# Kernel tuning notes

Measured on AMD Instinct MI355X. Metric: run time of the kernel, lower is better.

Reference implementation:

```python
import jax, jax.numpy as jnp
import numpy as np

VOCAB, EMB, HID = 128, 10, 20


def setup_inputs() -> dict:
    key = jax.random.key(0)
    ks = jax.random.split(key, 8)
    B, T = 256, 2048
    inputs = jax.random.randint(ks[0], (B, T), 0, VOCAB)
    s_emb = 1.0
    s_ih = 1.0 / np.sqrt(HID)  # torch RNN init: U(-1/sqrt(H), 1/sqrt(H))
    emb = jax.random.normal(ks[1], (VOCAB, EMB), dtype=jnp.float32)
    W_ih = jax.random.uniform(ks[2], (HID, EMB), jnp.float32, -s_ih, s_ih)
    W_hh = jax.random.uniform(ks[3], (HID, HID), jnp.float32, -s_ih, s_ih)
    b_ih = jax.random.uniform(ks[4], (HID,), jnp.float32, -s_ih, s_ih)
    b_hh = jax.random.uniform(ks[5], (HID,), jnp.float32, -s_ih, s_ih)
    s_out = 1.0 / np.sqrt(HID)
    W_out = jax.random.uniform(ks[6], (VOCAB, HID), jnp.float32, -s_out, s_out)
    b_out = jax.random.uniform(ks[7], (VOCAB,), jnp.float32, -s_out, s_out)
    return {"inputs": inputs, "emb": emb, "W_ih": W_ih, "W_hh": W_hh,
            "b_ih": b_ih, "b_hh": b_hh, "W_out": W_out, "b_out": b_out}


def reference(inputs, emb, W_ih, W_hh, b_ih, b_hh, W_out, b_out):
    # embedding lookup: [B, T, EMB]
    x = emb[inputs]
    B = x.shape[0]
    # precompute input contribution for all timesteps: [B, T, HID]
    xW = jnp.einsum('bte,he->bth', x, W_ih) + b_ih + b_hh
    xW_t = jnp.swapaxes(xW, 0, 1)  # [T, B, HID] for scan over time

    def step(h, xw_t):
        h = jnp.tanh(xw_t + h @ W_hh.T)
        return h, h

    h0 = jnp.zeros((B, HID), dtype=x.dtype)
    _, hs = jax.lax.scan(step, h0, xW_t)  # hs: [T, B, HID]
    hs = jnp.swapaxes(hs, 0, 1)  # [B, T, HID]
    # final linear projection: [B, T, VOCAB]
    return jnp.einsum('bth,vh->btv', hs, W_out) + b_out
```

## Files before the change

kernel.cpp:

```cpp
#include <hip/hip_runtime.h>

#define VOCAB 128
#define EMB   10
#define HID   20
#define BATCH 256
#define TLEN  2048
#define PRESCALE 2.8853900817779268f

__global__ __launch_bounds__(256)
void build_table(const float* __restrict__ emb, const float* __restrict__ W_ih,
                 const float* __restrict__ W_hh,
                 const float* __restrict__ b_ih, const float* __restrict__ b_hh,
                 float* __restrict__ P) {
    int idx = blockIdx.x * blockDim.x + threadIdx.x;
    if (idx < VOCAB * HID) {
        int v = idx / HID, j = idx % HID;
        float acc = b_ih[j] + b_hh[j];
        #pragma unroll
        for (int e = 0; e < EMB; ++e)
            acc = fmaf(W_ih[j * EMB + e], emb[v * EMB + e], acc);
        float wsum = 0.f;
        #pragma unroll
        for (int k = 0; k < HID; ++k) wsum += W_hh[j * HID + k];
        P[idx] = (acc + wsum) * PRESCALE;
    }
}

#define RNN_STEP(XW) { \
    const int ri_ = __float_as_int(r); \
    float bc[HID]; \
    _Pragma("unroll") \
    for (int k = 0; k < HID; ++k) \
        bc[k] = __int_as_float(__builtin_amdgcn_readlane(ri_, k)); \
    float a0 = (XW), a1 = 0.f, a2 = 0.f, a3 = 0.f; \
    _Pragma("unroll") \
    for (int k = 0; k < HID; k += 4) { \
        a0 = fmaf(w[k + 0], bc[k + 0], a0); \
        a1 = fmaf(w[k + 1], bc[k + 1], a1); \
        a2 = fmaf(w[k + 2], bc[k + 2], a2); \
        a3 = fmaf(w[k + 3], bc[k + 3], a3); } \
    float z_ = (a0 + a1) + (a2 + a3); \
    float u_ = __builtin_amdgcn_exp2f(z_); \
    r = __builtin_amdgcn_rcpf(u_ + 1.0f); }

__global__ __launch_bounds__(256)
void rnn_fused(const int* __restrict__ tokens, const float* __restrict__ W_hh,
               const float* __restrict__ P, const float* __restrict__ W_out,
               const float* __restrict__ b_out, float* __restrict__ out) {
    __shared__ float Pl[VOCAB * HID];
    __shared__ __align__(16) int tok[TLEN + 16];
    __shared__ float hbuf[2][64][64];
    const int tid  = threadIdx.x;
    const int lane = tid & 63;
    const int wid  = tid >> 6;
    const int b    = blockIdx.x;

    for (int i = tid; i < VOCAB * HID; i += 256) Pl[i] = P[i];
    const int4* src = (const int4*)(tokens + (size_t)b * TLEN);
    int4* dst = (int4*)tok;
    for (int i = tid; i < TLEN / 4; i += 256) dst[i] = src[i];
    if (tid < 16) tok[TLEN + tid] = 0;

    const int j = (lane & 31) < HID ? (lane & 31) : HID - 1;
    float w[HID], wB[HID];
    float bo0 = 0.f, bo1 = 0.f;
    if (wid == 0) {
        #pragma unroll
        for (int k = 0; k < HID; ++k)
            w[k] = W_hh[j * HID + k] * (-2.0f * PRESCALE);
    } else {
        const int v0 = 2 * lane, v1 = 2 * lane + 1;
        float s0 = 0.f, s1 = 0.f;
        #pragma unroll
        for (int k = 0; k < HID; ++k) {
            float wa = W_out[v0 * HID + k], wb = W_out[v1 * HID + k];
            s0 += wa; s1 += wb;
            w[k]  = -2.0f * wa;
            wB[k] = -2.0f * wb;
        }
        bo0 = b_out[v0] + s0; bo1 = b_out[v1] + s1;
    }
    __syncthreads();

    float r = 0.5f;
    int4 ta, tb, tkc, tkd;
    float xw0[4], xw1[4];
    if (wid == 0) {
        __builtin_amdgcn_s_setprio(1);
        ta  = *(const int4*)&tok[0];
        tb  = *(const int4*)&tok[4];
        tkc = *(const int4*)&tok[8];
        tkd = *(const int4*)&tok[12];
        xw0[0] = Pl[ta.x * HID + j]; xw0[1] = Pl[ta.y * HID + j];
        xw0[2] = Pl[ta.z * HID + j]; xw0[3] = Pl[ta.w * HID + j];
        xw1[0] = Pl[tb.x * HID + j]; xw1[1] = Pl[tb.y * HID + j];
        xw1[2] = Pl[tb.z * HID + j]; xw1[3] = Pl[tb.w * HID + j];
    }

    for (int c = 0; c < 33; ++c) {
        if (wid == 0 && c < 32) {
            float* hb = &hbuf[c & 1][0][lane];
            for (int t8 = 0; t8 < 64; t8 += 8) {
                const int t = c * 64 + t8;
                float* hrow = hb + t8 * 64;
                RNN_STEP(xw0[0]); hrow[0 * 64] = r;
                RNN_STEP(xw0[1]); hrow[1 * 64] = r;
                RNN_STEP(xw0[2]); hrow[2 * 64] = r;
                RNN_STEP(xw0[3]); hrow[3 * 64] = r;
                float n0[4] = {Pl[tkc.x * HID + j], Pl[tkc.y * HID + j],
                               Pl[tkc.z * HID + j], Pl[tkc.w * HID + j]};
                tkc = *(const int4*)&tok[t + 16];
                RNN_STEP(xw1[0]); hrow[4 * 64] = r;
                RNN_STEP(xw1[1]); hrow[5 * 64] = r;
                RNN_STEP(xw1[2]); hrow[6 * 64] = r;
                RNN_STEP(xw1[3]); hrow[7 * 64] = r;
                float n1[4] = {Pl[tkd.x * HID + j], Pl[tkd.y * HID + j],
                               Pl[tkd.z * HID + j], Pl[tkd.w * HID + j]};
                tkd = *(const int4*)&tok[t + 20];
                #pragma unroll
                for (int u = 0; u < 4; ++u) { xw0[u] = n0[u]; xw1[u] = n1[u]; }
            }
        }
        if (wid > 0 && c > 0) {
            const int cc = c - 1;
            const float* hb = &hbuf[cc & 1][0][0];
            float* outb = out + ((size_t)b * TLEN + (size_t)cc * 64) * VOCAB + 2 * lane;
            for (int rr = wid - 1; rr < 64; rr += 3) {
                const float* hr = hb + rr * 64;
                float a0 = bo0, a1 = bo1;
                #pragma unroll
                for (int k = 0; k < HID; k += 4) {
                    float4 hv = *(const float4*)(hr + k);
                    a0 = fmaf(hv.x, w[k + 0], a0); a1 = fmaf(hv.x, wB[k + 0], a1);
                    a0 = fmaf(hv.y, w[k + 1], a0); a1 = fmaf(hv.y, wB[k + 1], a1);
                    a0 = fmaf(hv.z, w[k + 2], a0); a1 = fmaf(hv.z, wB[k + 2], a1);
                    a0 = fmaf(hv.w, w[k + 3], a0); a1 = fmaf(hv.w, wB[k + 3], a1);
                }
                *(float2*)(outb + (size_t)rr * VOCAB) = make_float2(a0, a1);
            }
        }
        __syncthreads();
    }
}

extern "C" void kernel_launch(void* const* d_in, const int* in_sizes, int n_in,
                              void* d_out, int out_size, void* d_ws, size_t ws_size,
                              hipStream_t stream) {
    const int*   inputs = (const int*)  d_in[0];
    const float* emb    = (const float*)d_in[1];
    const float* W_ih   = (const float*)d_in[2];
    const float* W_hh   = (const float*)d_in[3];
    const float* b_ih   = (const float*)d_in[4];
    const float* b_hh   = (const float*)d_in[5];
    const float* W_out  = (const float*)d_in[6];
    const float* b_out  = (const float*)d_in[7];
    float* out = (float*)d_out;

    float* P = (float*)d_ws;

    build_table<<<(VOCAB * HID + 255) / 256, 256, 0, stream>>>(emb, W_ih, W_hh,
                                                               b_ih, b_hh, P);
    rnn_fused<<<BATCH, 256, 0, stream>>>(inputs, W_hh, P, W_out, b_out, out);
}
```

Baseline: 419.6 us.

## Process two batch rows per block with interleaved dual recurrence in one wave

Each block now handles two sequences. The recurrence wave runs both hidden-state chains interleaved in a single step macro: A is broadcast from lanes 0-19 and B from lanes 32-51. The projection waves cover 128 rows per chunk, and the grid is halved. The goal is to hide the serial step latency through instruction-level parallelism, at the cost of doubling per-step readlane and FMA work and leaving half of the CUs without a block.

```diff
diff --git a/kernel.cpp b/kernel.cpp
--- a/kernel.cpp
+++ b/kernel.cpp
@@ -26,42 +26,56 @@
     }
 }
 
-#define RNN_STEP(XW) { \
-    const int ri_ = __float_as_int(r); \
-    float bc[HID]; \
-    _Pragma("unroll") \
-    for (int k = 0; k < HID; ++k) \
-        bc[k] = __int_as_float(__builtin_amdgcn_readlane(ri_, k)); \
-    float a0 = (XW), a1 = 0.f, a2 = 0.f, a3 = 0.f; \
+#define RNN_STEP2(XWA, XWB) { \
+    const int riA_ = __float_as_int(rA); \
+    const int riB_ = __float_as_int(rB); \
+    float aA0 = (XWA), aA1 = 0.f, aA2 = 0.f, aA3 = 0.f; \
+    float aB0 = (XWB), aB1 = 0.f, aB2 = 0.f, aB3 = 0.f; \
     _Pragma("unroll") \
     for (int k = 0; k < HID; k += 4) { \
-        a0 = fmaf(w[k + 0], bc[k + 0], a0); \
-        a1 = fmaf(w[k + 1], bc[k + 1], a1); \
-        a2 = fmaf(w[k + 2], bc[k + 2], a2); \
-        a3 = fmaf(w[k + 3], bc[k + 3], a3); } \
-    float z_ = (a0 + a1) + (a2 + a3); \
-    float u_ = __builtin_amdgcn_exp2f(z_); \
-    r = __builtin_amdgcn_rcpf(u_ + 1.0f); }
+        float cA0 = __int_as_float(__builtin_amdgcn_readlane(riA_, k + 0)); \
+        float cB0 = __int_as_float(__builtin_amdgcn_readlane(riB_, 32 + k + 0)); \
+        float cA1 = __int_as_float(__builtin_amdgcn_readlane(riA_, k + 1)); \
+        float cB1 = __int_as_float(__builtin_amdgcn_readlane(riB_, 32 + k + 1)); \
+        float cA2 = __int_as_float(__builtin_amdgcn_readlane(riA_, k + 2)); \
+        float cB2 = __int_as_float(__builtin_amdgcn_readlane(riB_, 32 + k + 2)); \
+        float cA3 = __int_as_float(__builtin_amdgcn_readlane(riA_, k + 3)); \
+        float cB3 = __int_as_float(__builtin_amdgcn_readlane(riB_, 32 + k + 3)); \
+        aA0 = fmaf(w[k + 0], cA0, aA0); aB0 = fmaf(w[k + 0], cB0, aB0); \
+        aA1 = fmaf(w[k + 1], cA1, aA1); aB1 = fmaf(w[k + 1], cB1, aB1); \
+        aA2 = fmaf(w[k + 2], cA2, aA2); aB2 = fmaf(w[k + 2], cB2, aB2); \
+        aA3 = fmaf(w[k + 3], cA3, aA3); aB3 = fmaf(w[k + 3], cB3, aB3); } \
+    float zA_ = (aA0 + aA1) + (aA2 + aA3); \
+    float zB_ = (aB0 + aB1) + (aB2 + aB3); \
+    float uA_ = __builtin_amdgcn_exp2f(zA_); \
+    float uB_ = __builtin_amdgcn_exp2f(zB_); \
+    rA = __builtin_amdgcn_rcpf(uA_ + 1.0f); \
+    rB = __builtin_amdgcn_rcpf(uB_ + 1.0f); }
 
 __global__ __launch_bounds__(256)
 void rnn_fused(const int* __restrict__ tokens, const float* __restrict__ W_hh,
                const float* __restrict__ P, const float* __restrict__ W_out,
                const float* __restrict__ b_out, float* __restrict__ out) {
     __shared__ float Pl[VOCAB * HID];
-    __shared__ __align__(16) int tok[TLEN + 16];
+    __shared__ __align__(16) int tokA[TLEN + 16];
+    __shared__ __align__(16) int tokB[TLEN + 16];
     __shared__ float hbuf[2][64][64];
     const int tid  = threadIdx.x;
     const int lane = tid & 63;
     const int wid  = tid >> 6;
-    const int b    = blockIdx.x;
+    const int blk  = blockIdx.x;
+    const int bA   = 2 * blk, bB = 2 * blk + 1;
 
     for (int i = tid; i < VOCAB * HID; i += 256) Pl[i] = P[i];
-    const int4* src = (const int4*)(tokens + (size_t)b * TLEN);
-    int4* dst = (int4*)tok;
-    for (int i = tid; i < TLEN / 4; i += 256) dst[i] = src[i];
-    if (tid < 16) tok[TLEN + tid] = 0;
+    const int4* srcA = (const int4*)(tokens + (size_t)bA * TLEN);
+    const int4* srcB = (const int4*)(tokens + (size_t)bB * TLEN);
+    int4* dA = (int4*)tokA;
+    int4* dB = (int4*)tokB;
+    for (int i = tid; i < TLEN / 4; i += 256) { dA[i] = srcA[i]; dB[i] = srcB[i]; }
+    if (tid < 16) { tokA[TLEN + tid] = 0; tokB[TLEN + tid] = 0; }
 
     const int j = (lane & 31) < HID ? (lane & 31) : HID - 1;
+    const bool loHalf = lane < 32;
     float w[HID], wB[HID];
     float bo0 = 0.f, bo1 = 0.f;
     if (wid == 0) {
@@ -82,19 +96,23 @@
     }
     __syncthreads();
 
-    float r = 0.5f;
-    int4 ta, tb, tkc, tkd;
-    float xw0[4], xw1[4];
+    float rA = 0.5f, rB = 0.5f;
+    int4 taA, tbA, tcA, tdA, taB, tbB, tcB, tdB;
+    float xw0A[4], xw1A[4], xw0B[4], xw1B[4];
     if (wid == 0) {
         __builtin_amdgcn_s_setprio(1);
-        ta  = *(const int4*)&tok[0];
-        tb  = *(const int4*)&tok[4];
-        tkc = *(const int4*)&tok[8];
-        tkd = *(const int4*)&tok[12];
-        xw0[0] = Pl[ta.x * HID + j]; xw0[1] = Pl[ta.y * HID + j];
-        xw0[2] = Pl[ta.z * HID + j]; xw0[3] = Pl[ta.w * HID + j];
-        xw1[0] = Pl[tb.x * HID + j]; xw1[1] = Pl[tb.y * HID + j];
-        xw1[2] = Pl[tb.z * HID + j]; xw1[3] = Pl[tb.w * HID + j];
+        taA = *(const int4*)&tokA[0];  tbA = *(const int4*)&tokA[4];
+        tcA = *(const int4*)&tokA[8];  tdA = *(const int4*)&tokA[12];
+        taB = *(const int4*)&tokB[0];  tbB = *(const int4*)&tokB[4];
+        tcB = *(const int4*)&tokB[8];  tdB = *(const int4*)&tokB[12];
+        xw0A[0] = Pl[taA.x * HID + j]; xw0A[1] = Pl[taA.y * HID + j];
+        xw0A[2] = Pl[taA.z * HID + j]; xw0A[3] = Pl[taA.w * HID + j];
+        xw1A[0] = Pl[tbA.x * HID + j]; xw1A[1] = Pl[tbA.y * HID + j];
+        xw1A[2] = Pl[tbA.z * HID + j]; xw1A[3] = Pl[tbA.w * HID + j];
+        xw0B[0] = Pl[taB.x * HID + j]; xw0B[1] = Pl[taB.y * HID + j];
+        xw0B[2] = Pl[taB.z * HID + j]; xw0B[3] = Pl[taB.w * HID + j];
+        xw1B[0] = Pl[tbB.x * HID + j]; xw1B[1] = Pl[tbB.y * HID + j];
+        xw1B[2] = Pl[tbB.z * HID + j]; xw1B[3] = Pl[tbB.w * HID + j];
     }
 
     for (int c = 0; c < 33; ++c) {
@@ -103,30 +121,42 @@
             for (int t8 = 0; t8 < 64; t8 += 8) {
                 const int t = c * 64 + t8;
                 float* hrow = hb + t8 * 64;
-                RNN_STEP(xw0[0]); hrow[0 * 64] = r;
-                RNN_STEP(xw0[1]); hrow[1 * 64] = r;
-                RNN_STEP(xw0[2]); hrow[2 * 64] = r;
-                RNN_STEP(xw0[3]); hrow[3 * 64] = r;
-                float n0[4] = {Pl[tkc.x * HID + j], Pl[tkc.y * HID + j],
-                               Pl[tkc.z * HID + j], Pl[tkc.w * HID + j]};
-                tkc = *(const int4*)&tok[t + 16];
-                RNN_STEP(xw1[0]); hrow[4 * 64] = r;
-                RNN_STEP(xw1[1]); hrow[5 * 64] = r;
-                RNN_STEP(xw1[2]); hrow[6 * 64] = r;
-                RNN_STEP(xw1[3]); hrow[7 * 64] = r;
-                float n1[4] = {Pl[tkd.x * HID + j], Pl[tkd.y * HID + j],
-                               Pl[tkd.z * HID + j], Pl[tkd.w * HID + j]};
-                tkd = *(const int4*)&tok[t + 20];
+                RNN_STEP2(xw0A[0], xw0B[0]); hrow[0 * 64] = loHalf ? rA : rB;
+                RNN_STEP2(xw0A[1], xw0B[1]); hrow[1 * 64] = loHalf ? rA : rB;
+                RNN_STEP2(xw0A[2], xw0B[2]); hrow[2 * 64] = loHalf ? rA : rB;
+                RNN_STEP2(xw0A[3], xw0B[3]); hrow[3 * 64] = loHalf ? rA : rB;
+                float n0A[4] = {Pl[tcA.x * HID + j], Pl[tcA.y * HID + j],
+                                Pl[tcA.z * HID + j], Pl[tcA.w * HID + j]};
+                tcA = *(const int4*)&tokA[t + 16];
+                float n0B[4] = {Pl[tcB.x * HID + j], Pl[tcB.y * HID + j],
+                                Pl[tcB.z * HID + j], Pl[tcB.w * HID + j]};
+                tcB = *(const int4*)&tokB[t + 16];
+                RNN_STEP2(xw1A[0], xw1B[0]); hrow[4 * 64] = loHalf ? rA : rB;
+                RNN_STEP2(xw1A[1], xw1B[1]); hrow[5 * 64] = loHalf ? rA : rB;
+                RNN_STEP2(xw1A[2], xw1B[2]); hrow[6 * 64] = loHalf ? rA : rB;
+                RNN_STEP2(xw1A[3], xw1B[3]); hrow[7 * 64] = loHalf ? rA : rB;
+                float n1A[4] = {Pl[tdA.x * HID + j], Pl[tdA.y * HID + j],
+                                Pl[tdA.z * HID + j], Pl[tdA.w * HID + j]};
+                tdA = *(const int4*)&tokA[t + 20];
+                float n1B[4] = {Pl[tdB.x * HID + j], Pl[tdB.y * HID + j],
+                                Pl[tdB.z * HID + j], Pl[tdB.w * HID + j]};
+                tdB = *(const int4*)&tokB[t + 20];
                 #pragma unroll
-                for (int u = 0; u < 4; ++u) { xw0[u] = n0[u]; xw1[u] = n1[u]; }
+                for (int u = 0; u < 4; ++u) {
+                    xw0A[u] = n0A[u]; xw1A[u] = n1A[u];
+                    xw0B[u] = n0B[u]; xw1B[u] = n1B[u];
+                }
             }
         }
         if (wid > 0 && c > 0) {
             const int cc = c - 1;
-            const float* hb = &hbuf[cc & 1][0][0];
-            float* outb = out + ((size_t)b * TLEN + (size_t)cc * 64) * VOCAB + 2 * lane;
-            for (int rr = wid - 1; rr < 64; rr += 3) {
-                const float* hr = hb + rr * 64;
+            for (int rr = wid - 1; rr < 128; rr += 3) {
+                const int  row = rr & 63;
+                const bool isB = rr >= 64;
+                const float* hr = &hbuf[cc & 1][row][isB ? 32 : 0];
+                const int  bb  = isB ? bB : bA;
+                float* op = out + ((size_t)bb * TLEN + (size_t)cc * 64 + row) * VOCAB
+                                + 2 * lane;
                 float a0 = bo0, a1 = bo1;
                 #pragma unroll
                 for (int k = 0; k < HID; k += 4) {
@@ -136,7 +166,7 @@
                     a0 = fmaf(hv.z, w[k + 2], a0); a1 = fmaf(hv.z, wB[k + 2], a1);
                     a0 = fmaf(hv.w, w[k + 3], a0); a1 = fmaf(hv.w, wB[k + 3], a1);
                 }
-                *(float2*)(outb + (size_t)rr * VOCAB) = make_float2(a0, a1);
+                *(float2*)op = make_float2(a0, a1);
             }
         }
         __syncthreads();
@@ -160,5 +190,5 @@
 
     build_table<<<(VOCAB * HID + 255) / 256, 256, 0, stream>>>(emb, W_ih, W_hh,
                                                                b_ih, b_hh, P);
-    rnn_fused<<<BATCH, 256, 0, stream>>>(inputs, W_hh, P, W_out, b_out, out);
+    rnn_fused<<<BATCH / 2, 256, 0, stream>>>(inputs, W_hh, P, W_out, b_out, out);
 }
```

Measured after the change: 565.3 us. 34.7% more time.

## Pack two batch sequences per 512-thread block with shared consumer waves

Applied to the files above, without the earlier changes.

Each block now processes two batch rows, with two producer waves running the serial recurrences and six consumer waves computing output projections for both. The hidden-state buffers shrink to 32 columns per row, and only lanes below 32 write them. The grid halves to 128 blocks, so on a GPU with many CUs fewer CUs host the latency-bound recurrence, though each block gets more consumer waves per producer. This trades fewer resident blocks for sharing the shared-memory table load and balancing consumer work across the pair.

```diff
diff --git a/kernel.cpp b/kernel.cpp
--- a/kernel.cpp
+++ b/kernel.cpp
@@ -43,28 +43,35 @@
     float u_ = __builtin_amdgcn_exp2f(z_); \
     r = __builtin_amdgcn_rcpf(u_ + 1.0f); }
 
-__global__ __launch_bounds__(256)
+__global__ __launch_bounds__(512)
 void rnn_fused(const int* __restrict__ tokens, const float* __restrict__ W_hh,
                const float* __restrict__ P, const float* __restrict__ W_out,
                const float* __restrict__ b_out, float* __restrict__ out) {
     __shared__ float Pl[VOCAB * HID];
-    __shared__ __align__(16) int tok[TLEN + 16];
-    __shared__ float hbuf[2][64][64];
+    __shared__ __align__(16) int tokA[TLEN + 16];
+    __shared__ __align__(16) int tokB[TLEN + 16];
+    __shared__ float hbA[2 * 64 * 32];
+    __shared__ float hbB[2 * 64 * 32];
     const int tid  = threadIdx.x;
     const int lane = tid & 63;
     const int wid  = tid >> 6;
-    const int b    = blockIdx.x;
+    const int blk  = blockIdx.x;
+    const int bA   = 2 * blk, bB = 2 * blk + 1;
+    const bool isProd = (wid == 0) | (wid == 4);
 
-    for (int i = tid; i < VOCAB * HID; i += 256) Pl[i] = P[i];
-    const int4* src = (const int4*)(tokens + (size_t)b * TLEN);
-    int4* dst = (int4*)tok;
-    for (int i = tid; i < TLEN / 4; i += 256) dst[i] = src[i];
-    if (tid < 16) tok[TLEN + tid] = 0;
+    for (int i = tid; i < VOCAB * HID; i += 512) Pl[i] = P[i];
+    {
+        const int4* srcA = (const int4*)(tokens + (size_t)bA * TLEN);
+        const int4* srcB = (const int4*)(tokens + (size_t)bB * TLEN);
+        ((int4*)tokA)[tid] = srcA[tid];
+        ((int4*)tokB)[tid] = srcB[tid];
+    }
+    if (tid < 16) { tokA[TLEN + tid] = 0; tokB[TLEN + tid] = 0; }
 
-    const int j = (lane & 31) < HID ? (lane & 31) : HID - 1;
+    const int j = lane < HID ? lane : HID - 1;
     float w[HID], wB[HID];
     float bo0 = 0.f, bo1 = 0.f;
-    if (wid == 0) {
+    if (isProd) {
         #pragma unroll
         for (int k = 0; k < HID; ++k)
             w[k] = W_hh[j * HID + k] * (-2.0f * PRESCALE);
@@ -82,15 +89,17 @@
     }
     __syncthreads();
 
+    const int* tk     = (wid == 0) ? tokA : tokB;
+    float*     pbuf   = (wid == 0) ? hbA  : hbB;
     float r = 0.5f;
     int4 ta, tb, tkc, tkd;
     float xw0[4], xw1[4];
-    if (wid == 0) {
+    if (isProd) {
         __builtin_amdgcn_s_setprio(1);
-        ta  = *(const int4*)&tok[0];
-        tb  = *(const int4*)&tok[4];
-        tkc = *(const int4*)&tok[8];
-        tkd = *(const int4*)&tok[12];
+        ta  = *(const int4*)&tk[0];
+        tb  = *(const int4*)&tk[4];
+        tkc = *(const int4*)&tk[8];
+        tkd = *(const int4*)&tk[12];
         xw0[0] = Pl[ta.x * HID + j]; xw0[1] = Pl[ta.y * HID + j];
         xw0[2] = Pl[ta.z * HID + j]; xw0[3] = Pl[ta.w * HID + j];
         xw1[0] = Pl[tb.x * HID + j]; xw1[1] = Pl[tb.y * HID + j];
@@ -98,35 +107,40 @@
     }
 
     for (int c = 0; c < 33; ++c) {
-        if (wid == 0 && c < 32) {
-            float* hb = &hbuf[c & 1][0][lane];
+        if (isProd && c < 32) {
+            float* hb = pbuf + (c & 1) * (64 * 32) + lane;
             for (int t8 = 0; t8 < 64; t8 += 8) {
                 const int t = c * 64 + t8;
-                float* hrow = hb + t8 * 64;
-                RNN_STEP(xw0[0]); hrow[0 * 64] = r;
-                RNN_STEP(xw0[1]); hrow[1 * 64] = r;
-                RNN_STEP(xw0[2]); hrow[2 * 64] = r;
-                RNN_STEP(xw0[3]); hrow[3 * 64] = r;
+                float* hrow = hb + t8 * 32;
+                RNN_STEP(xw0[0]); if (lane < 32) hrow[0 * 32] = r;
+                RNN_STEP(xw0[1]); if (lane < 32) hrow[1 * 32] = r;
+                RNN_STEP(xw0[2]); if (lane < 32) hrow[2 * 32] = r;
+                RNN_STEP(xw0[3]); if (lane < 32) hrow[3 * 32] = r;
                 float n0[4] = {Pl[tkc.x * HID + j], Pl[tkc.y * HID + j],
                                Pl[tkc.z * HID + j], Pl[tkc.w * HID + j]};
-                tkc = *(const int4*)&tok[t + 16];
-                RNN_STEP(xw1[0]); hrow[4 * 64] = r;
-                RNN_STEP(xw1[1]); hrow[5 * 64] = r;
-                RNN_STEP(xw1[2]); hrow[6 * 64] = r;
-                RNN_STEP(xw1[3]); hrow[7 * 64] = r;
+                tkc = *(const int4*)&tk[t + 16];
+                RNN_STEP(xw1[0]); if (lane < 32) hrow[4 * 32] = r;
+                RNN_STEP(xw1[1]); if (lane < 32) hrow[5 * 32] = r;
+                RNN_STEP(xw1[2]); if (lane < 32) hrow[6 * 32] = r;
+                RNN_STEP(xw1[3]); if (lane < 32) hrow[7 * 32] = r;
                 float n1[4] = {Pl[tkd.x * HID + j], Pl[tkd.y * HID + j],
                                Pl[tkd.z * HID + j], Pl[tkd.w * HID + j]};
-                tkd = *(const int4*)&tok[t + 20];
+                tkd = *(const int4*)&tk[t + 20];
                 #pragma unroll
                 for (int u = 0; u < 4; ++u) { xw0[u] = n0[u]; xw1[u] = n1[u]; }
             }
         }
-        if (wid > 0 && c > 0) {
-            const int cc = c - 1;
-            const float* hb = &hbuf[cc & 1][0][0];
-            float* outb = out + ((size_t)b * TLEN + (size_t)cc * 64) * VOCAB + 2 * lane;
-            for (int rr = wid - 1; rr < 64; rr += 3) {
-                const float* hr = hb + rr * 64;
+        if (!isProd && c > 0) {
+            const int cc   = c - 1;
+            const int cwid = (wid < 4) ? wid - 1 : wid - 2;
+            const int boff = (cc & 1) * (64 * 32);
+            for (int rr = cwid; rr < 128; rr += 6) {
+                const int  row = rr & 63;
+                const bool isB = rr >= 64;
+                const float* hr = (isB ? hbB : hbA) + boff + row * 32;
+                const int  bb  = isB ? bB : bA;
+                float* op = out + ((size_t)bb * TLEN + (size_t)cc * 64 + row) * VOCAB
+                                + 2 * lane;
                 float a0 = bo0, a1 = bo1;
                 #pragma unroll
                 for (int k = 0; k < HID; k += 4) {
@@ -136,7 +150,7 @@
                     a0 = fmaf(hv.z, w[k + 2], a0); a1 = fmaf(hv.z, wB[k + 2], a1);
                     a0 = fmaf(hv.w, w[k + 3], a0); a1 = fmaf(hv.w, wB[k + 3], a1);
                 }
-                *(float2*)(outb + (size_t)rr * VOCAB) = make_float2(a0, a1);
+                *(float2*)op = make_float2(a0, a1);
             }
         }
         __syncthreads();
@@ -160,5 +174,5 @@
 
     build_table<<<(VOCAB * HID + 255) / 256, 256, 0, stream>>>(emb, W_ih, W_hh,
                                                                b_ih, b_hh, P);
-    rnn_fused<<<BATCH, 256, 0, stream>>>(inputs, W_hh, P, W_out, b_out, out);
+    rnn_fused<<<BATCH / 2, 512, 0, stream>>>(inputs, W_hh, P, W_out, b_out, out);
 }
```

After: 607.9 us. 44.9% more time.
